# Kernel tuning notes

Hardware: AMD Instinct MI355X
Metric: run time of the kernel (lower is better)

Reference implementation:

```python
import jax, jax.numpy as jnp
import numpy as np

B, T, C, H = 4, 2048, 1024, 16
HD = C // H  # head_dim = 64


def setup_inputs() -> dict:
    key = jax.random.key(0)
    k1, k2, k3 = jax.random.split(key, 3)
    x = jax.random.normal(k1, (B, T, C), dtype=jnp.float32)
    W_attn = jax.random.normal(k2, (C, 3 * C), dtype=jnp.float32) * 0.02
    W_proj = jax.random.normal(k3, (C, C), dtype=jnp.float32) * 0.02
    return {"x": x, "W_attn": W_attn, "W_proj": W_proj}


def reference(x, W_attn, W_proj):
    b, t, c = x.shape
    qkv = x @ W_attn                                  # (B,T,3C)
    q, k, v = jnp.split(qkv, 3, axis=-1)
    # (B,T,C) -> (B,H,T,HD)
    q = q.reshape(b, t, H, HD).transpose(0, 2, 1, 3)
    k = k.reshape(b, t, H, HD).transpose(0, 2, 1, 3)
    v = v.reshape(b, t, H, HD).transpose(0, 2, 1, 3)
    scale = jax.lax.rsqrt(jnp.asarray(HD, x.dtype))
    att = jnp.einsum('bhqd,bhkd->bhqk', q, k) * scale  # (B,H,T,T)
    # causal mask: positions where lower-triangular ones == 0 get -1e9 (replace, not add)
    causal = jnp.tril(jnp.ones((t, t), dtype=bool))
    att = jnp.where(causal[None, None], att, jnp.asarray(-1e9, x.dtype))
    att = jax.nn.softmax(att, axis=-1)
    y = jnp.einsum('bhqk,bhkd->bhqd', att, v)          # (B,H,T,HD)
    y = y.transpose(0, 2, 1, 3).reshape(b, t, c)
    return y @ W_proj
```

## Files before the change

### kernel.cpp

```cpp
#include <hip/hip_runtime.h>
#include <hip/hip_bf16.h>
#include <stdint.h>

#define BB 4
#define TT 2048
#define CC 1024
#define HH 16
#define HD 64
#define MM (BB*TT)
#define N1 (3*CC)

typedef short bf16x8 __attribute__((ext_vector_type(8)));
typedef float f32x4  __attribute__((ext_vector_type(4)));
typedef float f32x4v __attribute__((ext_vector_type(4)));
typedef uint32_t u32x2 __attribute__((ext_vector_type(2)));

using bf16 = __hip_bfloat16;

static __device__ __forceinline__ short f2bf(float f) {
  union { float f; uint32_t u; } v; v.f = f;
  uint32_t u = v.u;
  u += 0x7fffu + ((u >> 16) & 1u);
  return (short)(u >> 16);
}

static __device__ __forceinline__ uint32_t cvt_pk_bf16(float lo, float hi) {
  uint32_t r;
  asm("v_cvt_pk_bf16_f32 %0, %1, %2" : "=v"(r) : "v"(lo), "v"(hi));
  return r;
}

static __device__ __forceinline__ void gload_lds16(const void* g, void* l) {
  __builtin_amdgcn_global_load_lds(
      (const __attribute__((address_space(1))) uint32_t*)g,
      (__attribute__((address_space(3))) uint32_t*)l, 16, 0, 0);
}

__global__ __launch_bounds__(256) void xcast_kernel(const float* __restrict__ in,
                                                    bf16* __restrict__ out) {
  const int i = blockIdx.x * 256 + threadIdx.x;
  const float* ip = in + (size_t)i * 8;
  f32x4v f0 = ((const f32x4v*)ip)[0];
  f32x4v f1 = ((const f32x4v*)ip)[1];
  bf16x8 o;
#pragma unroll
  for (int j = 0; j < 4; ++j) { o[j] = f2bf(f0[j]); o[4 + j] = f2bf(f1[j]); }
  *(bf16x8*)((short*)out + (size_t)i * 8) = o;
}

__global__ __launch_bounds__(256) void wtrans_kernel(const float* __restrict__ in,
                                                     bf16* __restrict__ out,
                                                     int K, int N) {
  __shared__ float tl[32][33];
  const int bj = blockIdx.x, bi = blockIdx.y;
  const int tx = threadIdx.x, ty = threadIdx.y;
  const float* ip = in + (size_t)(bi * 32) * N + bj * 32;
#pragma unroll
  for (int r0 = 0; r0 < 4; ++r0) {
    int r = ty + r0 * 8;
    tl[r][tx] = ip[(size_t)r * N + tx];
  }
  __syncthreads();
  short* op = (short*)out + (size_t)(bj * 32) * K + bi * 32;
#pragma unroll
  for (int r0 = 0; r0 < 4; ++r0) {
    int r = ty + r0 * 8;
    op[(size_t)r * K + tx] = f2bf(tl[tx][r]);
  }
}

__global__ __launch_bounds__(256) void gemm_qkv_kernel(const bf16* __restrict__ xb,
                                                       const bf16* __restrict__ WaT,
                                                       bf16* __restrict__ qb,
                                                       bf16* __restrict__ kb,
                                                       bf16* __restrict__ vb) {
  __shared__ bf16 As[128 * 32];
  __shared__ bf16 Bs[128 * 32];
  const int tid = threadIdx.x;
  const int wid = tid >> 6, lane = tid & 63, row16 = lane & 15, g = lane >> 4;
  const int wr = wid >> 1, wc = wid & 1;
  const int mbase = blockIdx.x * 128, nbase = blockIdx.y * 128;

  f32x4 acc[4][4] = {};

  for (int kt = 0; kt < CC; kt += 32) {
#pragma unroll
    for (int i = 0; i < 2; ++i) {
      int chunk = i * 256 + tid;
      int row = chunk >> 2, c8 = (chunk & 3) * 8;
      gload_lds16(xb + (size_t)(mbase + row) * CC + kt + c8, (char*)As + chunk * 16);
      gload_lds16(WaT + (size_t)(nbase + row) * CC + kt + c8, (char*)Bs + chunk * 16);
    }
    __syncthreads();
    bf16x8 af[4], bfr[4];
#pragma unroll
    for (int m = 0; m < 4; ++m)
      af[m] = *(const bf16x8*)&As[(wr * 64 + m * 16 + row16) * 32 + g * 8];
#pragma unroll
    for (int n = 0; n < 4; ++n)
      bfr[n] = *(const bf16x8*)&Bs[(wc * 64 + n * 16 + row16) * 32 + g * 8];
#pragma unroll
    for (int m = 0; m < 4; ++m)
#pragma unroll
      for (int n = 0; n < 4; ++n)
        acc[m][n] = __builtin_amdgcn_mfma_f32_16x16x32_bf16(af[m], bfr[n], acc[m][n], 0, 0, 0);
    __syncthreads();
  }
#pragma unroll
  for (int m = 0; m < 4; ++m) {
    int grow0 = mbase + wr * 64 + m * 16 + g * 4;
#pragma unroll
    for (int n = 0; n < 4; ++n) {
      int gcol = nbase + wc * 64 + n * 16 + row16;
      int which = gcol >> 10, c = gcol & 1023, h = c >> 6, d = c & 63;
      short* dst = (short*)(which == 0 ? qb : (which == 1 ? kb : vb));
      float sc = (which == 0) ? 0.18033688011112042f : 1.0f;
#pragma unroll
      for (int r = 0; r < 4; ++r) {
        int rr = grow0 + r;
        int b = rr >> 11, t = rr & 2047;
        dst[(((size_t)(b * HH + h)) * TT + t) * HD + d] = f2bf(acc[m][n][r] * sc);
      }
    }
  }
}

__global__ __launch_bounds__(256, 2) void attn_kernel(const bf16* __restrict__ qb,
                                                      const bf16* __restrict__ kb,
                                                      const bf16* __restrict__ vb,
                                                      bf16* __restrict__ yb) {
  __shared__ __align__(16) char smem[65536];
  const int tid = threadIdx.x, wid = tid >> 6, lane = tid & 63;
  const int row16 = lane & 15, g = lane >> 4;
  const int pair = blockIdx.x, bh = blockIdx.y;
  const int Qlo = pair, Qhi = 15 - pair;
  const size_t hbase = (size_t)bh * TT * HD;
  const bf16* qh = qb + hbase;
  const char* kh = (const char*)(kb + hbase);
  const char* vh = (const char*)(vb + hbase);

  const int hq0 = Qhi * 128 + wid * 32;
  const int lq0 = Qlo * 128 + wid * 32;
  const int nt   = 2 * Qhi + 2;
  const int hcap = 2 * Qhi + (wid >> 1) + 1;
  const int lcap = 2 * Qlo + (wid >> 1) + 1;

  bf16x8 qfh[2][2], qfl[2][2];
#pragma unroll
  for (int m = 0; m < 2; ++m)
#pragma unroll
    for (int kk = 0; kk < 2; ++kk) {
      qfh[m][kk] = *(const bf16x8*)(qh + (size_t)(hq0 + m * 16 + row16) * HD + kk * 32 + g * 8);
      qfl[m][kk] = *(const bf16x8*)(qh + (size_t)(lq0 + m * 16 + row16) * HD + kk * 32 + g * 8);
    }

  f32x4 acch[2][4] = {}, accl[2][4] = {};
  float lph[2] = {0.f, 0.f}, lpl[2] = {0.f, 0.f};

  const int vkv0 = (tid >> 3) * 2, vd0 = (tid & 7) * 8;
  char* pw = smem + 32768 + wid * 8192;

  {
#pragma unroll
    for (int i = 0; i < 2; ++i) {
      int chunk = i * 256 + tid;
      int r = chunk >> 3;
      int cb = ((chunk & 7) * 16) ^ ((r & 7) << 4);
      gload_lds16(kh + (size_t)r * 128 + cb, smem + chunk * 16);
    }
    const char* vsrc = vh + (size_t)vkv0 * 128 + vd0 * 2;
    bf16x8 r0 = *(const bf16x8*)vsrc;
    bf16x8 r1 = *(const bf16x8*)(vsrc + 128);
    char* vdst = smem + 16384;
#pragma unroll
    for (int j = 0; j < 8; ++j) {
      int d = vd0 + j;
      uint32_t val = (uint32_t)(uint16_t)r0[j] | ((uint32_t)(uint16_t)r1[j] << 16);
      *(uint32_t*)(vdst + ((d * 128 + vkv0 * 2) ^ (((d + (d >> 3)) & 7) << 4))) = val;
    }
  }
  __syncthreads();

  for (int kt = 0; kt < nt; ++kt) {
    const int cur = kt & 1;
    char* kc = smem + cur * 8192;
    char* vc = smem + 16384 + cur * 8192;
    const bool havenext = (kt + 1 < nt);
    bf16x8 vr0, vr1;
    if (havenext) {
      char* kn = smem + (1 - cur) * 8192;
#pragma unroll
      for (int i = 0; i < 2; ++i) {
        int chunk = i * 256 + tid;
        int r = chunk >> 3;
        int cb = ((chunk & 7) * 16) ^ ((r & 7) << 4);
        gload_lds16(kh + (size_t)((kt + 1) * 64 + r) * 128 + cb, kn + chunk * 16);
      }
      const char* vsrc = vh + (size_t)((kt + 1) * 64 + vkv0) * 128 + vd0 * 2;
      vr0 = *(const bf16x8*)vsrc;
      vr1 = *(const bf16x8*)(vsrc + 128);
    }

    const bool hA = kt < hcap, lA = kt < lcap;
    if (hA | lA) {
      const bool maskh = (kt * 64 + 63) > hq0;
      const bool maskl = (kt * 64 + 63) > lq0;
#pragma unroll
      for (int c = 0; c < 4; ++c) {
        int krow = c * 16 + row16;
        int ksw = (krow & 7) << 4;
        bf16x8 kf0 = *(const bf16x8*)(kc + ((krow * 128 + g * 16) ^ ksw));
        bf16x8 kf1 = *(const bf16x8*)(kc + ((krow * 128 + 64 + g * 16) ^ ksw));
        if (hA) {
#pragma unroll
          for (int m = 0; m < 2; ++m) {
            f32x4 st = {};
            st = __builtin_amdgcn_mfma_f32_16x16x32_bf16(kf0, qfh[m][0], st, 0, 0, 0);
            st = __builtin_amdgcn_mfma_f32_16x16x32_bf16(kf1, qfh[m][1], st, 0, 0, 0);
            const int thr = hq0 + m * 16 + row16 - kt * 64;
            float pv[4];
#pragma unroll
            for (int r = 0; r < 4; ++r) {
              float pe = __builtin_amdgcn_exp2f(st[r]);
              if (maskh) pe = (c * 16 + g * 4 + r > thr) ? 0.f : pe;
              pv[r] = pe;
              lph[m] += pe;
            }
            u32x2 w;
            w[0] = cvt_pk_bf16(pv[0], pv[1]);
            w[1] = cvt_pk_bf16(pv[2], pv[3]);
            int prow = m * 16 + row16;
            *(u32x2*)(pw + ((prow * 128 + c * 32 + g * 8) ^ ((row16 & 7) << 4))) = w;
          }
        }
        if (lA) {
#pragma unroll
          for (int m = 0; m < 2; ++m) {
            f32x4 st = {};
            st = __builtin_amdgcn_mfma_f32_16x16x32_bf16(kf0, qfl[m][0], st, 0, 0, 0);
            st = __builtin_amdgcn_mfma_f32_16x16x32_bf16(kf1, qfl[m][1], st, 0, 0, 0);
            const int thr = lq0 + m * 16 + row16 - kt * 64;
            float pv[4];
#pragma unroll
            for (int r = 0; r < 4; ++r) {
              float pe = __builtin_amdgcn_exp2f(st[r]);
              if (maskl) pe = (c * 16 + g * 4 + r > thr) ? 0.f : pe;
              pv[r] = pe;
              lpl[m] += pe;
            }
            u32x2 w;
            w[0] = cvt_pk_bf16(pv[0], pv[1]);
            w[1] = cvt_pk_bf16(pv[2], pv[3]);
            int prow = m * 16 + row16;
            *(u32x2*)(pw + 4096 + ((prow * 128 + c * 32 + g * 8) ^ ((row16 & 7) << 4))) = w;
          }
        }
      }
      bf16x8 pah[2][2], pal[2][2];
#pragma unroll
      for (int m = 0; m < 2; ++m) {
        int prow = m * 16 + row16;
        int psw = (row16 & 7) << 4;
#pragma unroll
        for (int kk = 0; kk < 2; ++kk) {
          if (hA) pah[m][kk] = *(const bf16x8*)(pw + ((prow * 128 + kk * 64 + g * 16) ^ psw));
          if (lA) pal[m][kk] = *(const bf16x8*)(pw + 4096 + ((prow * 128 + kk * 64 + g * 16) ^ psw));
        }
      }
      __builtin_amdgcn_s_setprio(1);
#pragma unroll
      for (int nd = 0; nd < 4; ++nd) {
        int vrow = nd * 16 + row16;
        int vsw = ((vrow + (vrow >> 3)) & 7) << 4;
        bf16x8 vf0 = *(const bf16x8*)(vc + ((vrow * 128 + g * 16) ^ vsw));
        bf16x8 vf1 = *(const bf16x8*)(vc + ((vrow * 128 + 64 + g * 16) ^ vsw));
        if (hA) {
#pragma unroll
          for (int m = 0; m < 2; ++m) {
            acch[m][nd] = __builtin_amdgcn_mfma_f32_16x16x32_bf16(pah[m][0], vf0, acch[m][nd], 0, 0, 0);
            acch[m][nd] = __builtin_amdgcn_mfma_f32_16x16x32_bf16(pah[m][1], vf1, acch[m][nd], 0, 0, 0);
          }
        }
        if (lA) {
#pragma unroll
          for (int m = 0; m < 2; ++m) {
            accl[m][nd] = __builtin_amdgcn_mfma_f32_16x16x32_bf16(pal[m][0], vf0, accl[m][nd], 0, 0, 0);
            accl[m][nd] = __builtin_amdgcn_mfma_f32_16x16x32_bf16(pal[m][1], vf1, accl[m][nd], 0, 0, 0);
          }
        }
      }
      __builtin_amdgcn_s_setprio(0);
    }

    if (havenext) {
      char* vn = smem + 16384 + (1 - cur) * 8192;
#pragma unroll
      for (int j = 0; j < 8; ++j) {
        int d = vd0 + j;
        uint32_t val = (uint32_t)(uint16_t)vr0[j] | ((uint32_t)(uint16_t)vr1[j] << 16);
        *(uint32_t*)(vn + ((d * 128 + vkv0 * 2) ^ (((d + (d >> 3)) & 7) << 4))) = val;
      }
    }
    __syncthreads();
  }

  const int b = bh >> 4, h = bh & 15;
#pragma unroll
  for (int m = 0; m < 2; ++m) {
    lph[m] += __shfl_xor(lph[m], 16); lph[m] += __shfl_xor(lph[m], 32);
    lpl[m] += __shfl_xor(lpl[m], 16); lpl[m] += __shfl_xor(lpl[m], 32);
  }
#pragma unroll
  for (int m = 0; m < 2; ++m)
#pragma unroll
    for (int r = 0; r < 4; ++r) {
      int srcl = g * 4 + r;
      float lh = __shfl(lph[m], srcl);
      float ll = __shfl(lpl[m], srcl);
      float lih = __builtin_amdgcn_rcpf(lh);
      float lil = __builtin_amdgcn_rcpf(ll);
      int th = hq0 + m * 16 + g * 4 + r;
      int tl = lq0 + m * 16 + g * 4 + r;
#pragma unroll
      for (int nd = 0; nd < 4; ++nd) {
        ((short*)yb)[((size_t)(b * TT + th)) * CC + h * HD + nd * 16 + row16] =
            f2bf(acch[m][nd][r] * lih);
        ((short*)yb)[((size_t)(b * TT + tl)) * CC + h * HD + nd * 16 + row16] =
            f2bf(accl[m][nd][r] * lil);
      }
    }
}

__global__ __launch_bounds__(256) void gemm_proj_kernel(const bf16* __restrict__ yb,
                                                        const bf16* __restrict__ WpT,
                                                        float* __restrict__ out) {
  __shared__ bf16 As[128 * 32];
  __shared__ bf16 Bs[128 * 32];
  const int tid = threadIdx.x;
  const int wid = tid >> 6, lane = tid & 63, row16 = lane & 15, g = lane >> 4;
  const int wr = wid >> 1, wc = wid & 1;
  const int mbase = blockIdx.x * 128, nbase = blockIdx.y * 128;

  f32x4 acc[4][4] = {};

  for (int kt = 0; kt < CC; kt += 32) {
#pragma unroll
    for (int i = 0; i < 2; ++i) {
      int chunk = i * 256 + tid;
      int row = chunk >> 2, c8 = (chunk & 3) * 8;
      gload_lds16(yb + (size_t)(mbase + row) * CC + kt + c8, (char*)As + chunk * 16);
      gload_lds16(WpT + (size_t)(nbase + row) * CC + kt + c8, (char*)Bs + chunk * 16);
    }
    __syncthreads();
    bf16x8 af[4], bfr[4];
#pragma unroll
    for (int m = 0; m < 4; ++m)
      af[m] = *(const bf16x8*)&As[(wr * 64 + m * 16 + row16) * 32 + g * 8];
#pragma unroll
    for (int n = 0; n < 4; ++n)
      bfr[n] = *(const bf16x8*)&Bs[(wc * 64 + n * 16 + row16) * 32 + g * 8];
#pragma unroll
    for (int m = 0; m < 4; ++m)
#pragma unroll
      for (int n = 0; n < 4; ++n)
        acc[m][n] = __builtin_amdgcn_mfma_f32_16x16x32_bf16(af[m], bfr[n], acc[m][n], 0, 0, 0);
    __syncthreads();
  }
#pragma unroll
  for (int m = 0; m < 4; ++m) {
    int grow0 = mbase + wr * 64 + m * 16 + g * 4;
#pragma unroll
    for (int n = 0; n < 4; ++n) {
      int gcol = nbase + wc * 64 + n * 16 + row16;
#pragma unroll
      for (int r = 0; r < 4; ++r)
        out[(size_t)(grow0 + r) * CC + gcol] = acc[m][n][r];
    }
  }
}

extern "C" void kernel_launch(void* const* d_in, const int* in_sizes, int n_in,
                              void* d_out, int out_size, void* d_ws, size_t ws_size,
                              hipStream_t stream) {
  const float* x      = (const float*)d_in[0];
  const float* W_attn = (const float*)d_in[1];
  const float* W_proj = (const float*)d_in[2];
  float* out = (float*)d_out;

  char* ws = (char*)d_ws;
  bf16* WaT = (bf16*)(ws);
  bf16* WpT = (bf16*)(ws + 6291456);
  bf16* qb  = (bf16*)(ws + 8388608);
  bf16* kb  = (bf16*)(ws + 8388608 + 16777216);
  bf16* vb  = (bf16*)(ws + 8388608 + 2 * 16777216);
  bf16* yb  = (bf16*)(ws + 8388608 + 3 * 16777216);
  bf16* xbf = yb;

  xcast_kernel<<<dim3(MM * CC / (256 * 8)), 256, 0, stream>>>(x, xbf);
  wtrans_kernel<<<dim3(N1 / 32, CC / 32), dim3(32, 8), 0, stream>>>(W_attn, WaT, CC, N1);
  wtrans_kernel<<<dim3(CC / 32, CC / 32), dim3(32, 8), 0, stream>>>(W_proj, WpT, CC, CC);
  gemm_qkv_kernel<<<dim3(MM / 128, N1 / 128), 256, 0, stream>>>(xbf, WaT, qb, kb, vb);
  attn_kernel<<<dim3(8, BB * HH), 256, 0, stream>>>(qb, kb, vb, yb);
  gemm_proj_kernel<<<dim3(MM / 128, CC / 128), 256, 0, stream>>>(yb, WpT, out);
}
```

Baseline: 181.3 us.

## Feed softmax probabilities directly to 16x16x16 MFMA, skipping LDS round-trip

Attention P·V now uses the 16x16x16 bf16 MFMA, whose A-operand layout matches the S accumulator output. Probabilities are packed to bf16 in registers and consumed straight away, with no write to and reread from the per-wave LDS scratch. That halves shared memory per block, which could allow more resident blocks, and removes LDS traffic and waits. The cost is twice as many smaller MFMAs for P·V, each with a lower K per instruction, and narrower 8-byte V reads from LDS.

```diff
diff --git a/kernel.cpp b/kernel.cpp
--- a/kernel.cpp
+++ b/kernel.cpp
@@ -11,11 +11,22 @@
 #define N1 (3*CC)
 
 typedef short bf16x8 __attribute__((ext_vector_type(8)));
+typedef short s16x4  __attribute__((ext_vector_type(4)));
 typedef float f32x4  __attribute__((ext_vector_type(4)));
 typedef float f32x4v __attribute__((ext_vector_type(4)));
 typedef uint32_t u32x2 __attribute__((ext_vector_type(2)));
 
 using bf16 = __hip_bfloat16;
+
+#if __has_builtin(__builtin_amdgcn_mfma_f32_16x16x16bf16_1k)
+#define PV16(a, b, c) __builtin_amdgcn_mfma_f32_16x16x16bf16_1k(a, b, c, 0, 0, 0)
+#define HAVE_PV16 1
+#elif __has_builtin(__builtin_amdgcn_mfma_f32_16x16x16_bf16)
+#define PV16(a, b, c) __builtin_amdgcn_mfma_f32_16x16x16_bf16(a, b, c, 0, 0, 0)
+#define HAVE_PV16 1
+#else
+#define HAVE_PV16 0
+#endif
 
 static __device__ __forceinline__ short f2bf(float f) {
   union { float f; uint32_t u; } v; v.f = f;
@@ -129,7 +140,11 @@
                                                       const bf16* __restrict__ kb,
                                                       const bf16* __restrict__ vb,
                                                       bf16* __restrict__ yb) {
+#if HAVE_PV16
+  __shared__ __align__(16) char smem[32768];
+#else
   __shared__ __align__(16) char smem[65536];
+#endif
   const int tid = threadIdx.x, wid = tid >> 6, lane = tid & 63;
   const int row16 = lane & 15, g = lane >> 4;
   const int pair = blockIdx.x, bh = blockIdx.y;
@@ -158,7 +173,9 @@
   float lph[2] = {0.f, 0.f}, lpl[2] = {0.f, 0.f};
 
   const int vkv0 = (tid >> 3) * 2, vd0 = (tid & 7) * 8;
+#if !HAVE_PV16
   char* pw = smem + 32768 + wid * 8192;
+#endif
 
   {
 #pragma unroll
@@ -205,6 +222,74 @@
     if (hA | lA) {
       const bool maskh = (kt * 64 + 63) > hq0;
       const bool maskl = (kt * 64 + 63) > lq0;
+#if HAVE_PV16
+      __builtin_amdgcn_s_setprio(1);
+#pragma unroll
+      for (int c = 0; c < 4; ++c) {
+        int krow = c * 16 + row16;
+        int ksw = (krow & 7) << 4;
+        bf16x8 kf0 = *(const bf16x8*)(kc + ((krow * 128 + g * 16) ^ ksw));
+        bf16x8 kf1 = *(const bf16x8*)(kc + ((krow * 128 + 64 + g * 16) ^ ksw));
+        s16x4 pfh[2], pfl[2];
+        if (hA) {
+#pragma unroll
+          for (int m = 0; m < 2; ++m) {
+            f32x4 st = {};
+            st = __builtin_amdgcn_mfma_f32_16x16x32_bf16(kf0, qfh[m][0], st, 0, 0, 0);
+            st = __builtin_amdgcn_mfma_f32_16x16x32_bf16(kf1, qfh[m][1], st, 0, 0, 0);
+            const int thr = hq0 + m * 16 + row16 - kt * 64;
+            float pv[4];
+#pragma unroll
+            for (int r = 0; r < 4; ++r) {
+              float pe = __builtin_amdgcn_exp2f(st[r]);
+              if (maskh) pe = (c * 16 + g * 4 + r > thr) ? 0.f : pe;
+              pv[r] = pe;
+              lph[m] += pe;
+            }
+            u32x2 w;
+            w[0] = cvt_pk_bf16(pv[0], pv[1]);
+            w[1] = cvt_pk_bf16(pv[2], pv[3]);
+            pfh[m] = __builtin_bit_cast(s16x4, w);
+          }
+        }
+        if (lA) {
+#pragma unroll
+          for (int m = 0; m < 2; ++m) {
+            f32x4 st = {};
+            st = __builtin_amdgcn_mfma_f32_16x16x32_bf16(kf0, qfl[m][0], st, 0, 0, 0);
+            st = __builtin_amdgcn_mfma_f32_16x16x32_bf16(kf1, qfl[m][1], st, 0, 0, 0);
+            const int thr = lq0 + m * 16 + row16 - kt * 64;
+            float pv[4];
+#pragma unroll
+            for (int r = 0; r < 4; ++r) {
+              float pe = __builtin_amdgcn_exp2f(st[r]);
+              if (maskl) pe = (c * 16 + g * 4 + r > thr) ? 0.f : pe;
+              pv[r] = pe;
+              lpl[m] += pe;
+            }
+            u32x2 w;
+            w[0] = cvt_pk_bf16(pv[0], pv[1]);
+            w[1] = cvt_pk_bf16(pv[2], pv[3]);
+            pfl[m] = __builtin_bit_cast(s16x4, w);
+          }
+        }
+#pragma unroll
+        for (int nd = 0; nd < 4; ++nd) {
+          int vrow = nd * 16 + row16;
+          int vsw = ((vrow + (vrow >> 3)) & 7) << 4;
+          s16x4 vf = *(const s16x4*)(vc + ((vrow * 128 + c * 32 + g * 8) ^ vsw));
+          if (hA) {
+            acch[0][nd] = PV16(pfh[0], vf, acch[0][nd]);
+            acch[1][nd] = PV16(pfh[1], vf, acch[1][nd]);
+          }
+          if (lA) {
+            accl[0][nd] = PV16(pfl[0], vf, accl[0][nd]);
+            accl[1][nd] = PV16(pfl[1], vf, accl[1][nd]);
+          }
+        }
+      }
+      __builtin_amdgcn_s_setprio(0);
+#else
 #pragma unroll
       for (int c = 0; c < 4; ++c) {
         int krow = c * 16 + row16;
@@ -290,6 +375,7 @@
         }
       }
       __builtin_amdgcn_s_setprio(0);
+#endif
     }
 
     if (havenext) {
```

After: 188.9 us. +4.2%, slower.

## Keep softmax probabilities in registers and shrink attention tiles to 64 query rows

Applied to the files above, without the earlier changes.

The attention kernel now feeds the exp'd score fragments straight into a 16x16x16 bf16 MFMA for the PV product, so the per-wave LDS round trip for P goes away. That frees half of the shared memory. Query tiles shrink from 128 to 64 rows per block (16 per wave), the grid doubles to 16 pairs per head, and launch bounds allow 4 blocks per CU. The costs are twice as many PV MFMA instructions at the smaller K width, K/V tiles re-read from global by more blocks, and less register reuse per wave.

```diff
diff --git a/kernel.cpp b/kernel.cpp
--- a/kernel.cpp
+++ b/kernel.cpp
@@ -11,11 +11,14 @@
 #define N1 (3*CC)
 
 typedef short bf16x8 __attribute__((ext_vector_type(8)));
+typedef short s16x4  __attribute__((ext_vector_type(4)));
 typedef float f32x4  __attribute__((ext_vector_type(4)));
 typedef float f32x4v __attribute__((ext_vector_type(4)));
 typedef uint32_t u32x2 __attribute__((ext_vector_type(2)));
 
 using bf16 = __hip_bfloat16;
+
+#define PV16(a, b, c) __builtin_amdgcn_mfma_f32_16x16x16bf16_1k(a, b, c, 0, 0, 0)
 
 static __device__ __forceinline__ short f2bf(float f) {
   union { float f; uint32_t u; } v; v.f = f;
@@ -125,40 +128,36 @@
   }
 }
 
-__global__ __launch_bounds__(256, 2) void attn_kernel(const bf16* __restrict__ qb,
+__global__ __launch_bounds__(256, 4) void attn_kernel(const bf16* __restrict__ qb,
                                                       const bf16* __restrict__ kb,
                                                       const bf16* __restrict__ vb,
                                                       bf16* __restrict__ yb) {
-  __shared__ __align__(16) char smem[65536];
+  __shared__ __align__(16) char smem[32768];
   const int tid = threadIdx.x, wid = tid >> 6, lane = tid & 63;
   const int row16 = lane & 15, g = lane >> 4;
   const int pair = blockIdx.x, bh = blockIdx.y;
-  const int Qlo = pair, Qhi = 15 - pair;
+  const int Qhi = 31 - pair, Qlo = pair;
   const size_t hbase = (size_t)bh * TT * HD;
   const bf16* qh = qb + hbase;
   const char* kh = (const char*)(kb + hbase);
   const char* vh = (const char*)(vb + hbase);
 
-  const int hq0 = Qhi * 128 + wid * 32;
-  const int lq0 = Qlo * 128 + wid * 32;
-  const int nt   = 2 * Qhi + 2;
-  const int hcap = 2 * Qhi + (wid >> 1) + 1;
-  const int lcap = 2 * Qlo + (wid >> 1) + 1;
-
-  bf16x8 qfh[2][2], qfl[2][2];
-#pragma unroll
-  for (int m = 0; m < 2; ++m)
-#pragma unroll
-    for (int kk = 0; kk < 2; ++kk) {
-      qfh[m][kk] = *(const bf16x8*)(qh + (size_t)(hq0 + m * 16 + row16) * HD + kk * 32 + g * 8);
-      qfl[m][kk] = *(const bf16x8*)(qh + (size_t)(lq0 + m * 16 + row16) * HD + kk * 32 + g * 8);
-    }
-
-  f32x4 acch[2][4] = {}, accl[2][4] = {};
-  float lph[2] = {0.f, 0.f}, lpl[2] = {0.f, 0.f};
+  const int q0h = Qhi * 64 + wid * 16;
+  const int q0l = Qlo * 64 + wid * 16;
+  const int nt = Qhi + 1;
+  const int lcap = Qlo + 1;
+
+  bf16x8 qfh[2], qfl[2];
+#pragma unroll
+  for (int kk = 0; kk < 2; ++kk) {
+    qfh[kk] = *(const bf16x8*)(qh + (size_t)(q0h + row16) * HD + kk * 32 + g * 8);
+    qfl[kk] = *(const bf16x8*)(qh + (size_t)(q0l + row16) * HD + kk * 32 + g * 8);
+  }
+
+  f32x4 acch[4] = {}, accl[4] = {};
+  float lph = 0.f, lpl = 0.f;
 
   const int vkv0 = (tid >> 3) * 2, vd0 = (tid & 7) * 8;
-  char* pw = smem + 32768 + wid * 8192;
 
   {
 #pragma unroll
@@ -201,92 +200,61 @@
       vr1 = *(const bf16x8*)(vsrc + 128);
     }
 
-    const bool hA = kt < hcap, lA = kt < lcap;
-    if (hA | lA) {
-      const bool maskh = (kt * 64 + 63) > hq0;
-      const bool maskl = (kt * 64 + 63) > lq0;
+    {
+      const bool lA = kt < lcap;
+      const bool maskh = (kt == Qhi);
+      const bool maskl = (kt == Qlo);
+      const int thrh = q0h + row16 - kt * 64;
+      const int thrl = q0l + row16 - kt * 64;
+      __builtin_amdgcn_s_setprio(1);
 #pragma unroll
       for (int c = 0; c < 4; ++c) {
         int krow = c * 16 + row16;
         int ksw = (krow & 7) << 4;
         bf16x8 kf0 = *(const bf16x8*)(kc + ((krow * 128 + g * 16) ^ ksw));
         bf16x8 kf1 = *(const bf16x8*)(kc + ((krow * 128 + 64 + g * 16) ^ ksw));
-        if (hA) {
-#pragma unroll
-          for (int m = 0; m < 2; ++m) {
-            f32x4 st = {};
-            st = __builtin_amdgcn_mfma_f32_16x16x32_bf16(kf0, qfh[m][0], st, 0, 0, 0);
-            st = __builtin_amdgcn_mfma_f32_16x16x32_bf16(kf1, qfh[m][1], st, 0, 0, 0);
-            const int thr = hq0 + m * 16 + row16 - kt * 64;
-            float pv[4];
-#pragma unroll
-            for (int r = 0; r < 4; ++r) {
-              float pe = __builtin_amdgcn_exp2f(st[r]);
-              if (maskh) pe = (c * 16 + g * 4 + r > thr) ? 0.f : pe;
-              pv[r] = pe;
-              lph[m] += pe;
-            }
-            u32x2 w;
-            w[0] = cvt_pk_bf16(pv[0], pv[1]);
-            w[1] = cvt_pk_bf16(pv[2], pv[3]);
-            int prow = m * 16 + row16;
-            *(u32x2*)(pw + ((prow * 128 + c * 32 + g * 8) ^ ((row16 & 7) << 4))) = w;
+        s16x4 pfh, pfl;
+        {
+          f32x4 st = {};
+          st = __builtin_amdgcn_mfma_f32_16x16x32_bf16(kf0, qfh[0], st, 0, 0, 0);
+          st = __builtin_amdgcn_mfma_f32_16x16x32_bf16(kf1, qfh[1], st, 0, 0, 0);
+          float pv[4];
+#pragma unroll
+          for (int r = 0; r < 4; ++r) {
+            float pe = __builtin_amdgcn_exp2f(st[r]);
+            if (maskh) pe = (c * 16 + g * 4 + r > thrh) ? 0.f : pe;
+            pv[r] = pe;
+            lph += pe;
           }
+          u32x2 w;
+          w[0] = cvt_pk_bf16(pv[0], pv[1]);
+          w[1] = cvt_pk_bf16(pv[2], pv[3]);
+          pfh = __builtin_bit_cast(s16x4, w);
         }
         if (lA) {
-#pragma unroll
-          for (int m = 0; m < 2; ++m) {
-            f32x4 st = {};
-            st = __builtin_amdgcn_mfma_f32_16x16x32_bf16(kf0, qfl[m][0], st, 0, 0, 0);
-            st = __builtin_amdgcn_mfma_f32_16x16x32_bf16(kf1, qfl[m][1], st, 0, 0, 0);
-            const int thr = lq0 + m * 16 + row16 - kt * 64;
-            float pv[4];
-#pragma unroll
-            for (int r = 0; r < 4; ++r) {
-              float pe = __builtin_amdgcn_exp2f(st[r]);
-              if (maskl) pe = (c * 16 + g * 4 + r > thr) ? 0.f : pe;
-              pv[r] = pe;
-              lpl[m] += pe;
-            }
-            u32x2 w;
-            w[0] = cvt_pk_bf16(pv[0], pv[1]);
-            w[1] = cvt_pk_bf16(pv[2], pv[3]);
-            int prow = m * 16 + row16;
-            *(u32x2*)(pw + 4096 + ((prow * 128 + c * 32 + g * 8) ^ ((row16 & 7) << 4))) = w;
+          f32x4 st = {};
+          st = __builtin_amdgcn_mfma_f32_16x16x32_bf16(kf0, qfl[0], st, 0, 0, 0);
+          st = __builtin_amdgcn_mfma_f32_16x16x32_bf16(kf1, qfl[1], st, 0, 0, 0);
+          float pv[4];
+#pragma unroll
+          for (int r = 0; r < 4; ++r) {
+            float pe = __builtin_amdgcn_exp2f(st[r]);
+            if (maskl) pe = (c * 16 + g * 4 + r > thrl) ? 0.f : pe;
+            pv[r] = pe;
+            lpl += pe;
           }
+          u32x2 w;
+          w[0] = cvt_pk_bf16(pv[0], pv[1]);
+          w[1] = cvt_pk_bf16(pv[2], pv[3]);
+          pfl = __builtin_bit_cast(s16x4, w);
         }
-      }
-      bf16x8 pah[2][2], pal[2][2];
-#pragma unroll
-      for (int m = 0; m < 2; ++m) {
-        int prow = m * 16 + row16;
-        int psw = (row16 & 7) << 4;
-#pragma unroll
-        for (int kk = 0; kk < 2; ++kk) {
-          if (hA) pah[m][kk] = *(const bf16x8*)(pw + ((prow * 128 + kk * 64 + g * 16) ^ psw));
-          if (lA) pal[m][kk] = *(const bf16x8*)(pw + 4096 + ((prow * 128 + kk * 64 + g * 16) ^ psw));
-        }
-      }
-      __builtin_amdgcn_s_setprio(1);
-#pragma unroll
-      for (int nd = 0; nd < 4; ++nd) {
-        int vrow = nd * 16 + row16;
-        int vsw = ((vrow + (vrow >> 3)) & 7) << 4;
-        bf16x8 vf0 = *(const bf16x8*)(vc + ((vrow * 128 + g * 16) ^ vsw));
-        bf16x8 vf1 = *(const bf16x8*)(vc + ((vrow * 128 + 64 + g * 16) ^ vsw));
-        if (hA) {
-#pragma unroll
-          for (int m = 0; m < 2; ++m) {
-            acch[m][nd] = __builtin_amdgcn_mfma_f32_16x16x32_bf16(pah[m][0], vf0, acch[m][nd], 0, 0, 0);
-            acch[m][nd] = __builtin_amdgcn_mfma_f32_16x16x32_bf16(pah[m][1], vf1, acch[m][nd], 0, 0, 0);
-          }
-        }
-        if (lA) {
-#pragma unroll
-          for (int m = 0; m < 2; ++m) {
-            accl[m][nd] = __builtin_amdgcn_mfma_f32_16x16x32_bf16(pal[m][0], vf0, accl[m][nd], 0, 0, 0);
-            accl[m][nd] = __builtin_amdgcn_mfma_f32_16x16x32_bf16(pal[m][1], vf1, accl[m][nd], 0, 0, 0);
-          }
+#pragma unroll
+        for (int nd = 0; nd < 4; ++nd) {
+          int vrow = nd * 16 + row16;
+          int vsw = ((vrow + (vrow >> 3)) & 7) << 4;
+          s16x4 vf = *(const s16x4*)(vc + ((vrow * 128 + c * 32 + g * 8) ^ vsw));
+          acch[nd] = PV16(pfh, vf, acch[nd]);
+          if (lA) accl[nd] = PV16(pfl, vf, accl[nd]);
         }
       }
       __builtin_amdgcn_s_setprio(0);
@@ -305,30 +273,25 @@
   }
 
   const int b = bh >> 4, h = bh & 15;
-#pragma unroll
-  for (int m = 0; m < 2; ++m) {
-    lph[m] += __shfl_xor(lph[m], 16); lph[m] += __shfl_xor(lph[m], 32);
-    lpl[m] += __shfl_xor(lpl[m], 16); lpl[m] += __shfl_xor(lpl[m], 32);
-  }
-#pragma unroll
-  for (int m = 0; m < 2; ++m)
-#pragma unroll
-    for (int r = 0; r < 4; ++r) {
-      int srcl = g * 4 + r;
-      float lh = __shfl(lph[m], srcl);
-      float ll = __shfl(lpl[m], srcl);
-      float lih = __builtin_amdgcn_rcpf(lh);
-      float lil = __builtin_amdgcn_rcpf(ll);
-      int th = hq0 + m * 16 + g * 4 + r;
-      int tl = lq0 + m * 16 + g * 4 + r;
-#pragma unroll
-      for (int nd = 0; nd < 4; ++nd) {
-        ((short*)yb)[((size_t)(b * TT + th)) * CC + h * HD + nd * 16 + row16] =
-            f2bf(acch[m][nd][r] * lih);
-        ((short*)yb)[((size_t)(b * TT + tl)) * CC + h * HD + nd * 16 + row16] =
-            f2bf(accl[m][nd][r] * lil);
-      }
-    }
+  lph += __shfl_xor(lph, 16); lph += __shfl_xor(lph, 32);
+  lpl += __shfl_xor(lpl, 16); lpl += __shfl_xor(lpl, 32);
+#pragma unroll
+  for (int r = 0; r < 4; ++r) {
+    int srcl = g * 4 + r;
+    float lh = __shfl(lph, srcl);
+    float ll = __shfl(lpl, srcl);
+    float lih = __builtin_amdgcn_rcpf(lh);
+    float lil = __builtin_amdgcn_rcpf(ll);
+    int th = q0h + g * 4 + r;
+    int tl = q0l + g * 4 + r;
+#pragma unroll
+    for (int nd = 0; nd < 4; ++nd) {
+      ((short*)yb)[((size_t)(b * TT + th)) * CC + h * HD + nd * 16 + row16] =
+          f2bf(acch[nd][r] * lih);
+      ((short*)yb)[((size_t)(b * TT + tl)) * CC + h * HD + nd * 16 + row16] =
+          f2bf(accl[nd][r] * lil);
+    }
+  }
 }
 
 __global__ __launch_bounds__(256) void gemm_proj_kernel(const bf16* __restrict__ yb,
@@ -400,6 +363,6 @@
   wtrans_kernel<<<dim3(N1 / 32, CC / 32), dim3(32, 8), 0, stream>>>(W_attn, WaT, CC, N1);
   wtrans_kernel<<<dim3(CC / 32, CC / 32), dim3(32, 8), 0, stream>>>(W_proj, WpT, CC, CC);
   gemm_qkv_kernel<<<dim3(MM / 128, N1 / 128), 256, 0, stream>>>(xbf, WaT, qb, kb, vb);
-  attn_kernel<<<dim3(8, BB * HH), 256, 0, stream>>>(qb, kb, vb, yb);
+  attn_kernel<<<dim3(16, BB * HH), 256, 0, stream>>>(qb, kb, vb, yb);
   gemm_proj_kernel<<<dim3(MM / 128, CC / 128), 256, 0, stream>>>(yb, WpT, out);
 }
```

New measurement: 231.9 us. 1.28x slower.

## Split high/low query processing to share one P buffer and raise occupancy

Applied to the files above, without the earlier changes.

The attention loop now processes the high and low query tiles one after the other instead of interleaved. This lets both tiles reuse a single 4KB per-wave P staging buffer, shrinking shared memory from 64KB to 48KB and raising launch bounds to 3 blocks per CU. The aim is more resident waves to hide latency. In exchange it gives up the interleaved MFMA streams that gave ILP within a wave, re-reads K fragments from LDS for each tile, and tightens the register budget.

```diff
diff --git a/kernel.cpp b/kernel.cpp
--- a/kernel.cpp
+++ b/kernel.cpp
@@ -125,11 +125,11 @@
   }
 }
 
-__global__ __launch_bounds__(256, 2) void attn_kernel(const bf16* __restrict__ qb,
+__global__ __launch_bounds__(256, 3) void attn_kernel(const bf16* __restrict__ qb,
                                                       const bf16* __restrict__ kb,
                                                       const bf16* __restrict__ vb,
                                                       bf16* __restrict__ yb) {
-  __shared__ __align__(16) char smem[65536];
+  __shared__ __align__(16) char smem[49152];
   const int tid = threadIdx.x, wid = tid >> 6, lane = tid & 63;
   const int row16 = lane & 15, g = lane >> 4;
   const int pair = blockIdx.x, bh = blockIdx.y;
@@ -158,7 +158,7 @@
   float lph[2] = {0.f, 0.f}, lpl[2] = {0.f, 0.f};
 
   const int vkv0 = (tid >> 3) * 2, vd0 = (tid & 7) * 8;
-  char* pw = smem + 32768 + wid * 8192;
+  char* pw = smem + 32768 + wid * 4096;
 
   {
 #pragma unroll
@@ -202,70 +202,44 @@
     }
 
     const bool hA = kt < hcap, lA = kt < lcap;
-    if (hA | lA) {
+    const int psw = (row16 & 7) << 4;
+
+    if (hA) {
       const bool maskh = (kt * 64 + 63) > hq0;
-      const bool maskl = (kt * 64 + 63) > lq0;
 #pragma unroll
       for (int c = 0; c < 4; ++c) {
         int krow = c * 16 + row16;
         int ksw = (krow & 7) << 4;
         bf16x8 kf0 = *(const bf16x8*)(kc + ((krow * 128 + g * 16) ^ ksw));
         bf16x8 kf1 = *(const bf16x8*)(kc + ((krow * 128 + 64 + g * 16) ^ ksw));
-        if (hA) {
-#pragma unroll
-          for (int m = 0; m < 2; ++m) {
-            f32x4 st = {};
-            st = __builtin_amdgcn_mfma_f32_16x16x32_bf16(kf0, qfh[m][0], st, 0, 0, 0);
-            st = __builtin_amdgcn_mfma_f32_16x16x32_bf16(kf1, qfh[m][1], st, 0, 0, 0);
-            const int thr = hq0 + m * 16 + row16 - kt * 64;
-            float pv[4];
-#pragma unroll
-            for (int r = 0; r < 4; ++r) {
-              float pe = __builtin_amdgcn_exp2f(st[r]);
-              if (maskh) pe = (c * 16 + g * 4 + r > thr) ? 0.f : pe;
-              pv[r] = pe;
-              lph[m] += pe;
-            }
-            u32x2 w;
-            w[0] = cvt_pk_bf16(pv[0], pv[1]);
-            w[1] = cvt_pk_bf16(pv[2], pv[3]);
-            int prow = m * 16 + row16;
-            *(u32x2*)(pw + ((prow * 128 + c * 32 + g * 8) ^ ((row16 & 7) << 4))) = w;
+#pragma unroll
+        for (int m = 0; m < 2; ++m) {
+          f32x4 st = {};
+          st = __builtin_amdgcn_mfma_f32_16x16x32_bf16(kf0, qfh[m][0], st, 0, 0, 0);
+          st = __builtin_amdgcn_mfma_f32_16x16x32_bf16(kf1, qfh[m][1], st, 0, 0, 0);
+          const int thr = hq0 + m * 16 + row16 - kt * 64;
+          float pv[4];
+#pragma unroll
+          for (int r = 0; r < 4; ++r) {
+            float pe = __builtin_amdgcn_exp2f(st[r]);
+            if (maskh) pe = (c * 16 + g * 4 + r > thr) ? 0.f : pe;
+            pv[r] = pe;
+            lph[m] += pe;
           }
+          u32x2 w;
+          w[0] = cvt_pk_bf16(pv[0], pv[1]);
+          w[1] = cvt_pk_bf16(pv[2], pv[3]);
+          int prow = m * 16 + row16;
+          *(u32x2*)(pw + ((prow * 128 + c * 32 + g * 8) ^ psw)) = w;
         }
-        if (lA) {
-#pragma unroll
-          for (int m = 0; m < 2; ++m) {
-            f32x4 st = {};
-            st = __builtin_amdgcn_mfma_f32_16x16x32_bf16(kf0, qfl[m][0], st, 0, 0, 0);
-            st = __builtin_amdgcn_mfma_f32_16x16x32_bf16(kf1, qfl[m][1], st, 0, 0, 0);
-            const int thr = lq0 + m * 16 + row16 - kt * 64;
-            float pv[4];
-#pragma unroll
-            for (int r = 0; r < 4; ++r) {
-              float pe = __builtin_amdgcn_exp2f(st[r]);
-              if (maskl) pe = (c * 16 + g * 4 + r > thr) ? 0.f : pe;
-              pv[r] = pe;
-              lpl[m] += pe;
-            }
-            u32x2 w;
-            w[0] = cvt_pk_bf16(pv[0], pv[1]);
-            w[1] = cvt_pk_bf16(pv[2], pv[3]);
-            int prow = m * 16 + row16;
-            *(u32x2*)(pw + 4096 + ((prow * 128 + c * 32 + g * 8) ^ ((row16 & 7) << 4))) = w;
-          }
-        }
-      }
-      bf16x8 pah[2][2], pal[2][2];
+      }
+      bf16x8 pa[2][2];
 #pragma unroll
       for (int m = 0; m < 2; ++m) {
         int prow = m * 16 + row16;
-        int psw = (row16 & 7) << 4;
-#pragma unroll
-        for (int kk = 0; kk < 2; ++kk) {
-          if (hA) pah[m][kk] = *(const bf16x8*)(pw + ((prow * 128 + kk * 64 + g * 16) ^ psw));
-          if (lA) pal[m][kk] = *(const bf16x8*)(pw + 4096 + ((prow * 128 + kk * 64 + g * 16) ^ psw));
-        }
+#pragma unroll
+        for (int kk = 0; kk < 2; ++kk)
+          pa[m][kk] = *(const bf16x8*)(pw + ((prow * 128 + kk * 64 + g * 16) ^ psw));
       }
       __builtin_amdgcn_s_setprio(1);
 #pragma unroll
@@ -274,19 +248,63 @@
         int vsw = ((vrow + (vrow >> 3)) & 7) << 4;
         bf16x8 vf0 = *(const bf16x8*)(vc + ((vrow * 128 + g * 16) ^ vsw));
         bf16x8 vf1 = *(const bf16x8*)(vc + ((vrow * 128 + 64 + g * 16) ^ vsw));
-        if (hA) {
-#pragma unroll
-          for (int m = 0; m < 2; ++m) {
-            acch[m][nd] = __builtin_amdgcn_mfma_f32_16x16x32_bf16(pah[m][0], vf0, acch[m][nd], 0, 0, 0);
-            acch[m][nd] = __builtin_amdgcn_mfma_f32_16x16x32_bf16(pah[m][1], vf1, acch[m][nd], 0, 0, 0);
+#pragma unroll
+        for (int m = 0; m < 2; ++m) {
+          acch[m][nd] = __builtin_amdgcn_mfma_f32_16x16x32_bf16(pa[m][0], vf0, acch[m][nd], 0, 0, 0);
+          acch[m][nd] = __builtin_amdgcn_mfma_f32_16x16x32_bf16(pa[m][1], vf1, acch[m][nd], 0, 0, 0);
+        }
+      }
+      __builtin_amdgcn_s_setprio(0);
+    }
+
+    if (lA) {
+      const bool maskl = (kt * 64 + 63) > lq0;
+#pragma unroll
+      for (int c = 0; c < 4; ++c) {
+        int krow = c * 16 + row16;
+        int ksw = (krow & 7) << 4;
+        bf16x8 kf0 = *(const bf16x8*)(kc + ((krow * 128 + g * 16) ^ ksw));
+        bf16x8 kf1 = *(const bf16x8*)(kc + ((krow * 128 + 64 + g * 16) ^ ksw));
+#pragma unroll
+        for (int m = 0; m < 2; ++m) {
+          f32x4 st = {};
+          st = __builtin_amdgcn_mfma_f32_16x16x32_bf16(kf0, qfl[m][0], st, 0, 0, 0);
+          st = __builtin_amdgcn_mfma_f32_16x16x32_bf16(kf1, qfl[m][1], st, 0, 0, 0);
+          const int thr = lq0 + m * 16 + row16 - kt * 64;
+          float pv[4];
+#pragma unroll
+          for (int r = 0; r < 4; ++r) {
+            float pe = __builtin_amdgcn_exp2f(st[r]);
+            if (maskl) pe = (c * 16 + g * 4 + r > thr) ? 0.f : pe;
+            pv[r] = pe;
+            lpl[m] += pe;
           }
+          u32x2 w;
+          w[0] = cvt_pk_bf16(pv[0], pv[1]);
+          w[1] = cvt_pk_bf16(pv[2], pv[3]);
+          int prow = m * 16 + row16;
+          *(u32x2*)(pw + ((prow * 128 + c * 32 + g * 8) ^ psw)) = w;
         }
-        if (lA) {
-#pragma unroll
-          for (int m = 0; m < 2; ++m) {
-            accl[m][nd] = __builtin_amdgcn_mfma_f32_16x16x32_bf16(pal[m][0], vf0, accl[m][nd], 0, 0, 0);
-            accl[m][nd] = __builtin_amdgcn_mfma_f32_16x16x32_bf16(pal[m][1], vf1, accl[m][nd], 0, 0, 0);
-          }
+      }
+      bf16x8 pa[2][2];
+#pragma unroll
+      for (int m = 0; m < 2; ++m) {
+        int prow = m * 16 + row16;
+#pragma unroll
+        for (int kk = 0; kk < 2; ++kk)
+          pa[m][kk] = *(const bf16x8*)(pw + ((prow * 128 + kk * 64 + g * 16) ^ psw));
+      }
+      __builtin_amdgcn_s_setprio(1);
+#pragma unroll
+      for (int nd = 0; nd < 4; ++nd) {
+        int vrow = nd * 16 + row16;
+        int vsw = ((vrow + (vrow >> 3)) & 7) << 4;
+        bf16x8 vf0 = *(const bf16x8*)(vc + ((vrow * 128 + g * 16) ^ vsw));
+        bf16x8 vf1 = *(const bf16x8*)(vc + ((vrow * 128 + 64 + g * 16) ^ vsw));
+#pragma unroll
+        for (int m = 0; m < 2; ++m) {
+          accl[m][nd] = __builtin_amdgcn_mfma_f32_16x16x32_bf16(pa[m][0], vf0, accl[m][nd], 0, 0, 0);
+          accl[m][nd] = __builtin_amdgcn_mfma_f32_16x16x32_bf16(pa[m][1], vf1, accl[m][nd], 0, 0, 0);
         }
       }
       __builtin_amdgcn_s_setprio(0);
```

Measured after the change: 318.1 us. 75.4% more time.
